# Performance work log

Measured on AMD Instinct MI355X. Metric: run time of the kernel, lower is better.

## Reference

```python
import math
import jax, jax.numpy as jnp
import numpy as np

B, L = 64, 25
FEAT, HEADS, LAYERS = 128, 8, 2
USER_N, POI_N, CAT_N = 5000, 10000, 400


def _autocorr(q, k, v):
    # q,k,v: [B,L,H,E] ; training-mode AutoCorrelation (self.training=True)
    Lq = q.shape[1]
    qp = jnp.transpose(q, (0, 2, 3, 1))  # [B,H,E,L]
    kp = jnp.transpose(k, (0, 2, 3, 1))
    vp = jnp.transpose(v, (0, 2, 3, 1))
    qf = jnp.fft.rfft(qp, axis=-1)
    kf = jnp.fft.rfft(kp, axis=-1)
    corr = jnp.fft.irfft(qf * jnp.conj(kf), n=Lq, axis=-1)  # [B,H,E,L]
    top_k = int(1 * math.log(Lq))  # factor=1 -> 3 for L=25
    mean_value = corr.mean(axis=(1, 2))  # [B,L]
    _, index = jax.lax.top_k(mean_value.mean(axis=0), top_k)  # [K], shared across batch
    weights = mean_value[:, index]  # [B,K]
    tmp_corr = jax.nn.softmax(weights, axis=-1)
    # roll(values, -delay) == gather at (t + delay) mod L
    gidx = (jnp.arange(Lq)[None, :] + index[:, None]) % Lq  # [K,L]
    patterns = vp[..., gidx]  # [B,H,E,K,L]
    agg = jnp.einsum('bhekl,bk->bhel', patterns, tmp_corr)  # weighted delay aggregation
    return jnp.transpose(agg, (0, 3, 1, 2))  # [B,L,H,E]


def _ac_layer(qx, kx, vx, w, b):
    # w: [4, d, d] torch-layout [out,in] for (q,k,v,out) projections; b: [4, d]
    Bq, Lq, d = qx.shape
    q = (qx @ w[0].T + b[0]).reshape(Bq, Lq, HEADS, -1)
    k = (kx @ w[1].T + b[1]).reshape(Bq, kx.shape[1], HEADS, -1)
    v = (vx @ w[2].T + b[2]).reshape(Bq, vx.shape[1], HEADS, -1)
    out = _autocorr(q, k, v).reshape(Bq, Lq, -1)
    return out @ w[3].T + b[3]


def setup_inputs() -> dict:
    key = jax.random.key(0)
    ks = jax.random.split(key, 16)
    d = FEAT
    inp = {
        'user': jax.random.randint(ks[0], (B, L), 0, USER_N),
        'poi': jax.random.randint(ks[1], (B, L), 0, POI_N),
        'cat': jax.random.randint(ks[2], (B, L), 0, CAT_N),
        'lat': jax.random.normal(ks[3], (B, L), jnp.float32),
        'lon': jax.random.normal(ks[4], (B, L), jnp.float32),
        'tod': jax.random.randint(ks[5], (B, L), 0, 24),
        'dow': jax.random.randint(ks[6], (B, L), 0, 7),
        'unixtime': jax.random.normal(ks[7], (B, L), jnp.float32),
        'user_emb': jax.random.normal(ks[8], (USER_N, d), jnp.float32) * 0.02,
        'poi_emb': jax.random.normal(ks[9], (POI_N, d), jnp.float32) * 0.02,
        'cat_emb': jax.random.normal(ks[10], (CAT_N, d), jnp.float32) * 0.02,
        'tod_emb': jax.random.normal(ks[11], (24, d), jnp.float32) * 0.02,
        'dow_emb': jax.random.normal(ks[12], (7, d), jnp.float32) * 0.02,
        'user_embc': jax.random.normal(jax.random.fold_in(ks[8], 1), (USER_N, d), jnp.float32) * 0.02,
        'tod_embc': jax.random.normal(jax.random.fold_in(ks[11], 1), (24, d), jnp.float32) * 0.02,
        'dow_embc': jax.random.normal(jax.random.fold_in(ks[12], 1), (7, d), jnp.float32) * 0.02,
        # W[layer, module(poi,cat,xpoi,xcat), proj(q,k,v,o), out, in]
        'W': jax.random.normal(ks[13], (LAYERS, 4, 4, d, d), jnp.float32) * (1.0 / math.sqrt(d)),
        'Bv': jnp.zeros((LAYERS, 4, 4, d), jnp.float32),
        'value_w': jax.random.normal(ks[14], (1, L), jnp.float32) * 0.1,
        'value_b': jnp.zeros((1,), jnp.float32),
        'distance_matrix': jax.random.uniform(ks[15], (POI_N, POI_N), jnp.float32) * 10.0,
    }
    return inp


def reference(user, poi, cat, lat, lon, tod, dow, unixtime,
              user_emb, poi_emb, cat_emb, tod_emb, dow_emb,
              user_embc, tod_embc, dow_embc,
              W, Bv, value_w, value_b, distance_matrix):
    x = user_emb[user] + poi_emb[poi] + tod_emb[tod] + dow_emb[dow]        # [B,L,d]
    xc = user_embc[user] + cat_emb[cat] + tod_embc[tod] + dow_embc[dow]   # [B,L,d]

    interval_dis = distance_matrix[poi]  # [B,L,P] row gather == index_select loop
    interval = jnp.exp(-interval_dis / (interval_dis.max() - interval_dis.min()))

    out, outc = x, xc
    for i in range(LAYERS):
        out = _ac_layer(out, out, out, W[i, 0], Bv[i, 0])
        outc = _ac_layer(outc, outc, outc, W[i, 1], Bv[i, 1])
        out = _ac_layer(out, outc, outc, W[i, 2], Bv[i, 2])
        outc = _ac_layer(outc, out, out, W[i, 3], Bv[i, 3])

    attn = jnp.einsum('pd,bld->bpl', poi_emb, out) * jnp.transpose(interval, (0, 2, 1))
    attn_cat = jnp.einsum('cd,bld->bcl', cat_emb, outc)
    pre_poi = (attn @ value_w.T + value_b)[..., 0]      # [B,P]
    pre_cat = (attn_cat @ value_w.T + value_b)[..., 0]  # [B,C]
    return pre_poi, pre_cat
```

## Files before the change

kernel.cpp:

```cpp
#include <hip/hip_runtime.h>
#include <hip/hip_bf16.h>

#define BB 64
#define LL 25
#define DD 128
#define BL 1600
#define POI_N 10000
#define CAT_N 400

__global__ __launch_bounds__(256) void embed_kernel(
    const int* __restrict__ user, const int* __restrict__ poi, const int* __restrict__ cat,
    const int* __restrict__ tod, const int* __restrict__ dow,
    const float* __restrict__ ue, const float* __restrict__ pe, const float* __restrict__ ce,
    const float* __restrict__ te, const float* __restrict__ de,
    const float* __restrict__ uec, const float* __restrict__ tec, const float* __restrict__ dec,
    float* __restrict__ x, float* __restrict__ xc, unsigned* __restrict__ mm)
{
    int idx = blockIdx.x * 256 + threadIdx.x;
    if (idx == 0) { mm[0] = 0u; mm[1] = 0x7f7fffffu; }
    int bl = idx >> 7, d = idx & 127;
    int u = user[bl], p = poi[bl], c = cat[bl], td = tod[bl], dw = dow[bl];
    x[idx]  = ue[u * DD + d] + pe[p * DD + d] + te[td * DD + d] + de[dw * DD + d];
    xc[idx] = uec[u * DD + d] + ce[c * DD + d] + tec[td * DD + d] + dec[dw * DD + d];
}

__global__ __launch_bounds__(256) void minmax_kernel(
    const int* __restrict__ poi, const float* __restrict__ Dm, unsigned* __restrict__ mm)
{
    int bl = blockIdx.x;
    const float4* r = (const float4*)(Dm + (size_t)poi[bl] * POI_N);
    float mx = -1e30f, mn = 1e30f;
    for (int i = threadIdx.x; i < POI_N / 4; i += 256) {
        float4 v4 = r[i];
        mx = fmaxf(mx, fmaxf(fmaxf(v4.x, v4.y), fmaxf(v4.z, v4.w)));
        mn = fminf(mn, fminf(fminf(v4.x, v4.y), fminf(v4.z, v4.w)));
    }
    for (int off = 32; off > 0; off >>= 1) {
        mx = fmaxf(mx, __shfl_down(mx, off));
        mn = fminf(mn, __shfl_down(mn, off));
    }
    __shared__ float smx[4], smn[4];
    int lid = threadIdx.x & 63, wid = threadIdx.x >> 6;
    if (lid == 0) { smx[wid] = mx; smn[wid] = mn; }
    __syncthreads();
    if (threadIdx.x == 0) {
        mx = fmaxf(fmaxf(smx[0], smx[1]), fmaxf(smx[2], smx[3]));
        mn = fminf(fminf(smn[0], smn[1]), fminf(smn[2], smn[3]));
        atomicMax(&mm[0], __float_as_uint(mx));
        atomicMin(&mm[1], __float_as_uint(mn));
    }
}

__global__ __launch_bounds__(256) void proj_kernel(
    const float* __restrict__ sq, const float* __restrict__ sk, const float* __restrict__ sv,
    const float* __restrict__ Wbase, const float* __restrict__ Bbase,
    float* __restrict__ q, float* __restrict__ k, float* __restrict__ v)
{
    int r = blockIdx.y;
    const float* src = (r == 0) ? sq : (r == 1 ? sk : sv);
    float* dst       = (r == 0) ? q  : (r == 1 ? k  : v);
    const float* Wm   = Wbase + r * DD * DD;
    const float* bias = Bbase + r * DD;
    int mbase = blockIdx.x * 32;
    __shared__ float sS[32][132];
    __shared__ float sWc[128][68];
    int t = threadIdx.x;

    for (int i = t; i < 32 * 32; i += 256) {
        int m = i >> 5, c = (i & 31) << 2;
        *(float4*)&sS[m][c] = *(const float4*)(src + (mbase + m) * DD + c);
    }
    __syncthreads();

    int nh = t & 31, mg = t >> 5;
    float acc[4][4] = {};
    for (int kb = 0; kb < 128; kb += 64) {
        for (int i = t; i < 128 * 16; i += 256) {
            int n = i >> 4, c = (i & 15) << 2;
            *(float4*)&sWc[n][c] = *(const float4*)(Wm + n * DD + kb + c);
        }
        __syncthreads();
#pragma unroll 4
        for (int kk = 0; kk < 64; kk += 4) {
            float4 a[4], w[4];
#pragma unroll
            for (int i2 = 0; i2 < 4; i2++) a[i2] = *(const float4*)&sS[mg * 4 + i2][kb + kk];
#pragma unroll
            for (int j = 0; j < 4; j++) w[j] = *(const float4*)&sWc[nh + 32 * j][kk];
#pragma unroll
            for (int i2 = 0; i2 < 4; i2++)
#pragma unroll
                for (int j = 0; j < 4; j++)
                    acc[i2][j] += a[i2].x * w[j].x + a[i2].y * w[j].y +
                                  a[i2].z * w[j].z + a[i2].w * w[j].w;
        }
        __syncthreads();
    }
#pragma unroll
    for (int i2 = 0; i2 < 4; i2++) {
        int m = mbase + mg * 4 + i2;
#pragma unroll
        for (int j = 0; j < 4; j++) {
            int n = nh + 32 * j;
            dst[m * DD + n] = acc[i2][j] + bias[n];
        }
    }
}

__global__ __launch_bounds__(256) void corr_kernel(
    const float* __restrict__ q, const float* __restrict__ k, float* __restrict__ mv)
{
    int b = blockIdx.x;
    __shared__ float sq[LL * DD], sk[LL * DD];
    __shared__ float rbuf[LL][4];
    int t = threadIdx.x;
    for (int i = t; i < 800; i += 256) {
        int c = i << 2;
        *(float4*)&sq[c] = *(const float4*)(q + b * LL * DD + c);
        *(float4*)&sk[c] = *(const float4*)(k + b * LL * DD + c);
    }
    __syncthreads();
    int lid = t & 63, wid = t >> 6;
    for (int tau = 0; tau < LL; tau++) {
        float s = 0.f;
        for (int e = t; e < LL * DD; e += 256) {
            int srow = e >> 7, d = e & 127;
            int qrow = srow + tau; if (qrow >= LL) qrow -= LL;
            s += sq[qrow * DD + d] * sk[e];
        }
        for (int off = 32; off > 0; off >>= 1) s += __shfl_down(s, off);
        if (lid == 0) rbuf[tau][wid] = s;
    }
    __syncthreads();
    if (t < LL)
        mv[b * LL + t] = (rbuf[t][0] + rbuf[t][1] + rbuf[t][2] + rbuf[t][3]) * (1.0f / 128.0f);
}

__global__ void topsm_kernel(const float* __restrict__ mv, float* __restrict__ tc,
                             int* __restrict__ idxout)
{
    __shared__ float sbm[LL];
    __shared__ int sidx[3];
    int t = threadIdx.x;
    if (t < LL) {
        float s = 0.f;
        for (int b = 0; b < BB; b++) s += mv[b * LL + t];
        sbm[t] = s;
    }
    __syncthreads();
    if (t == 0) {
        float loc[LL];
        for (int i = 0; i < LL; i++) loc[i] = sbm[i];
        for (int j = 0; j < 3; j++) {
            int bi = 0; float bvv = loc[0];
            for (int i = 1; i < LL; i++) if (loc[i] > bvv) { bvv = loc[i]; bi = i; }
            sidx[j] = bi; idxout[j] = bi; loc[bi] = -1e30f;
        }
    }
    __syncthreads();
    if (t < BB) {
        float w0 = mv[t * LL + sidx[0]];
        float w1 = mv[t * LL + sidx[1]];
        float w2 = mv[t * LL + sidx[2]];
        float m = fmaxf(w0, fmaxf(w1, w2));
        float e0 = expf(w0 - m), e1 = expf(w1 - m), e2 = expf(w2 - m);
        float inv = 1.0f / (e0 + e1 + e2);
        tc[t * 4 + 0] = e0 * inv; tc[t * 4 + 1] = e1 * inv; tc[t * 4 + 2] = e2 * inv;
    }
}

__global__ __launch_bounds__(256) void aggproj_kernel(
    const float* __restrict__ v, const float* __restrict__ tc, const int* __restrict__ idx3,
    const float* __restrict__ Wm, const float* __restrict__ bias, float* __restrict__ dst)
{
    int mbase = blockIdx.x * 32;
    __shared__ float sS[32][132];
    __shared__ float sWc[128][68];
    int t = threadIdx.x;
    int i0 = idx3[0], i1 = idx3[1], i2x = idx3[2];

    for (int i = t; i < 32 * 32; i += 256) {
        int m = i >> 5, c = (i & 31) << 2;
        int row = mbase + m;
        int b = row / LL, l = row - b * LL;
        int l0 = l + i0;  if (l0 >= LL) l0 -= LL;
        int l1 = l + i1;  if (l1 >= LL) l1 -= LL;
        int l2 = l + i2x; if (l2 >= LL) l2 -= LL;
        float w0 = tc[b * 4 + 0], w1 = tc[b * 4 + 1], w2 = tc[b * 4 + 2];
        float4 v0 = *(const float4*)(v + (b * LL + l0) * DD + c);
        float4 v1 = *(const float4*)(v + (b * LL + l1) * DD + c);
        float4 v2 = *(const float4*)(v + (b * LL + l2) * DD + c);
        float4 a;
        a.x = w0 * v0.x + w1 * v1.x + w2 * v2.x;
        a.y = w0 * v0.y + w1 * v1.y + w2 * v2.y;
        a.z = w0 * v0.z + w1 * v1.z + w2 * v2.z;
        a.w = w0 * v0.w + w1 * v1.w + w2 * v2.w;
        *(float4*)&sS[m][c] = a;
    }
    __syncthreads();

    int nh = t & 31, mg = t >> 5;
    float acc[4][4] = {};
    for (int kb = 0; kb < 128; kb += 64) {
        for (int i = t; i < 128 * 16; i += 256) {
            int n = i >> 4, c = (i & 15) << 2;
            *(float4*)&sWc[n][c] = *(const float4*)(Wm + n * DD + kb + c);
        }
        __syncthreads();
#pragma unroll 4
        for (int kk = 0; kk < 64; kk += 4) {
            float4 a[4], w[4];
#pragma unroll
            for (int ii = 0; ii < 4; ii++) a[ii] = *(const float4*)&sS[mg * 4 + ii][kb + kk];
#pragma unroll
            for (int j = 0; j < 4; j++) w[j] = *(const float4*)&sWc[nh + 32 * j][kk];
#pragma unroll
            for (int ii = 0; ii < 4; ii++)
#pragma unroll
                for (int j = 0; j < 4; j++)
                    acc[ii][j] += a[ii].x * w[j].x + a[ii].y * w[j].y +
                                  a[ii].z * w[j].z + a[ii].w * w[j].w;
        }
        __syncthreads();
    }
#pragma unroll
    for (int ii = 0; ii < 4; ii++) {
        int m = mbase + mg * 4 + ii;
#pragma unroll
        for (int j = 0; j < 4; j++) {
            int n = nh + 32 * j;
            dst[m * DD + n] = acc[ii][j] + bias[n];
        }
    }
}

__global__ __launch_bounds__(256) void precat_kernel(
    const float* __restrict__ outc, const float* __restrict__ cat_emb,
    const float* __restrict__ vw, const float* __restrict__ vbp, float* __restrict__ dstc)
{
    int b = blockIdx.x, t = threadIdx.x;
    __shared__ float y[DD];
    __shared__ float svw[LL];
    if (t < LL) svw[t] = vw[t];
    __syncthreads();
    if (t < DD) {
        float s = 0.f;
        for (int l = 0; l < LL; l++) s += svw[l] * outc[(b * LL + l) * DD + t];
        y[t] = s;
    }
    __syncthreads();
    float vb = vbp[0];
    for (int c = t; c < CAT_N; c += 256) {
        float s = 0.f;
        for (int d = 0; d < DD; d += 4) {
            float4 ce4 = *(const float4*)(cat_emb + c * DD + d);
            s += ce4.x * y[d] + ce4.y * y[d + 1] + ce4.z * y[d + 2] + ce4.w * y[d + 3];
        }
        dstc[b * CAT_N + c] = s + vb;
    }
}

__global__ __launch_bounds__(256) void prepoi_kernel(
    const float* __restrict__ outp, const float* __restrict__ poi_emb,
    const int* __restrict__ poi_idx, const float* __restrict__ Dm,
    const unsigned* __restrict__ mm, const float* __restrict__ vw,
    const float* __restrict__ vbp, float* __restrict__ dstp)
{
    int b = blockIdx.y;
    int pbase = blockIdx.x << 7;
    __shared__ float sO[LL][132];
    __shared__ float sPc[128][68];
    __shared__ float sS[LL][132];
    __shared__ float svw[LL];
    __shared__ int srow[LL];
    __shared__ float red[128];
    int t = threadIdx.x;

    for (int i = t; i < 800; i += 256) {
        int l = i >> 5, c = (i & 31) << 2;
        *(float4*)&sO[l][c] = *(const float4*)(outp + (b * LL + l) * DD + c);
    }
    if (t < LL) { svw[t] = vw[t]; srow[t] = poi_idx[b * LL + t]; }
    __syncthreads();

    int nh = t & 31, mg = t >> 5;
    float acc[4][4] = {};
    for (int kb = 0; kb < 128; kb += 64) {
        for (int i = t; i < 128 * 16; i += 256) {
            int p = i >> 4, c = (i & 15) << 2;
            float4 val = {0.f, 0.f, 0.f, 0.f};
            if (pbase + p < POI_N) val = *(const float4*)(poi_emb + (pbase + p) * DD + kb + c);
            *(float4*)&sPc[p][c] = val;
        }
        __syncthreads();
#pragma unroll 4
        for (int kk = 0; kk < 64; kk += 4) {
            float4 a0 = *(const float4*)&sO[mg][kb + kk];
            float4 a1 = *(const float4*)&sO[mg + 8][kb + kk];
            float4 a2 = *(const float4*)&sO[mg + 16][kb + kk];
            float4 a3 = {0.f, 0.f, 0.f, 0.f};
            if (mg == 0) a3 = *(const float4*)&sO[24][kb + kk];
#pragma unroll
            for (int j = 0; j < 4; j++) {
                float4 p4 = *(const float4*)&sPc[nh + 32 * j][kk];
                acc[j][0] += p4.x * a0.x + p4.y * a0.y + p4.z * a0.z + p4.w * a0.w;
                acc[j][1] += p4.x * a1.x + p4.y * a1.y + p4.z * a1.z + p4.w * a1.w;
                acc[j][2] += p4.x * a2.x + p4.y * a2.y + p4.z * a2.z + p4.w * a2.w;
                acc[j][3] += p4.x * a3.x + p4.y * a3.y + p4.z * a3.z + p4.w * a3.w;
            }
        }
        __syncthreads();
    }
#pragma unroll
    for (int j = 0; j < 4; j++) {
        int pl = nh + 32 * j;
        sS[mg][pl]      = acc[j][0];
        sS[mg + 8][pl]  = acc[j][1];
        sS[mg + 16][pl] = acc[j][2];
        if (mg == 0) sS[24][pl] = acc[j][3];
    }
    __syncthreads();

    float gmax = __uint_as_float(mm[0]);
    float gmin = __uint_as_float(mm[1]);
    float ninv = -1.0f / (gmax - gmin);
    int pp = t & 127, half = t >> 7;
    int p = pbase + pp;
    float s = 0.f;
    if (p < POI_N) {
        int l0 = half ? 13 : 0, l1 = half ? 25 : 13;
        for (int l = l0; l < l1; l++) {
            float dv = Dm[(size_t)srow[l] * POI_N + p];
            s += svw[l] * expf(dv * ninv) * sS[l][pp];
        }
    }
    if (half) red[pp] = s;
    __syncthreads();
    if (!half && p < POI_N)
        dstp[(size_t)b * POI_N + p] = s + red[pp] + vbp[0];
}

extern "C" void kernel_launch(void* const* d_in, const int* in_sizes, int n_in,
                              void* d_out, int out_size, void* d_ws, size_t ws_size,
                              hipStream_t stream)
{
    const int*   user = (const int*)d_in[0];
    const int*   poi  = (const int*)d_in[1];
    const int*   cat  = (const int*)d_in[2];
    const int*   tod  = (const int*)d_in[5];
    const int*   dow  = (const int*)d_in[6];
    const float* ue   = (const float*)d_in[8];
    const float* pe   = (const float*)d_in[9];
    const float* ce   = (const float*)d_in[10];
    const float* te   = (const float*)d_in[11];
    const float* de   = (const float*)d_in[12];
    const float* uec  = (const float*)d_in[13];
    const float* tec  = (const float*)d_in[14];
    const float* dec  = (const float*)d_in[15];
    const float* W    = (const float*)d_in[16];
    const float* Bv   = (const float*)d_in[17];
    const float* vw   = (const float*)d_in[18];
    const float* vb   = (const float*)d_in[19];
    const float* Dm   = (const float*)d_in[20];

    float* ws = (float*)d_ws;
    float* O0 = ws;
    float* C0 = ws + 204800;
    float* O1 = ws + 409600;
    float* C1 = ws + 614400;
    float* Q  = ws + 819200;
    float* Kb = ws + 1024000;
    float* V  = ws + 1228800;
    float* MV = ws + 1433600;
    float* TC = ws + 1435200;
    int*   IDX = (int*)(ws + 1435456);
    unsigned* MM = (unsigned*)(ws + 1435460);

    float* out_poi = (float*)d_out;
    float* out_cat = out_poi + BB * POI_N;

    embed_kernel<<<800, 256, 0, stream>>>(user, poi, cat, tod, dow,
                                          ue, pe, ce, te, de, uec, tec, dec, O0, C0, MM);
    minmax_kernel<<<BL, 256, 0, stream>>>(poi, Dm, MM);

    auto ac = [&](const float* qx, const float* kx, const float* vx, int i, int j, float* dstbuf) {
        const float* Wb = W + (size_t)((i * 4 + j) * 4) * DD * DD;
        const float* Bb = Bv + (size_t)((i * 4 + j) * 4) * DD;
        proj_kernel<<<dim3(50, 3), 256, 0, stream>>>(qx, kx, vx, Wb, Bb, Q, Kb, V);
        corr_kernel<<<BB, 256, 0, stream>>>(Q, Kb, MV);
        topsm_kernel<<<1, 256, 0, stream>>>(MV, TC, IDX);
        aggproj_kernel<<<50, 256, 0, stream>>>(V, TC, IDX, Wb + 3 * DD * DD, Bb + 3 * DD, dstbuf);
    };

    ac(O0, O0, O0, 0, 0, O1);
    ac(C0, C0, C0, 0, 1, C1);
    ac(O1, C1, C1, 0, 2, O0);
    ac(C1, O0, O0, 0, 3, C0);
    ac(O0, O0, O0, 1, 0, O1);
    ac(C0, C0, C0, 1, 1, C1);
    ac(O1, C1, C1, 1, 2, O0);
    ac(C1, O0, O0, 1, 3, C0);

    precat_kernel<<<BB, 256, 0, stream>>>(C0, ce, vw, vb, out_cat);
    prepoi_kernel<<<dim3(79, BB), 256, 0, stream>>>(O0, pe, poi, Dm, MM, vw, vb, out_poi);
}
```

Measured before the change: 1.201 ms.

## Fuse autocorrelation layer into two per-batch kernels and run independent layers concurrently

Replaces the four-kernel sequence per autocorrelation layer (projection, correlation, top-k/softmax, aggregation+output projection) with two per-batch kernels. The first computes Q and K in shared memory, does the circular correlation and accumulates the batch-mean via atomics. The second does top-k and softmax per block, projects V in shared memory, aggregates and applies the output projection. The two independent layers (out and outc paths) are launched together via a second grid dimension. This removes launches and global Q/K/V round-trips, but each block recomputes the top-k, and the atomic float sums make the ordering nondeterministic.

```diff
diff --git a/kernel.cpp b/kernel.cpp
--- a/kernel.cpp
+++ b/kernel.cpp
@@ -14,9 +14,11 @@
     const float* __restrict__ ue, const float* __restrict__ pe, const float* __restrict__ ce,
     const float* __restrict__ te, const float* __restrict__ de,
     const float* __restrict__ uec, const float* __restrict__ tec, const float* __restrict__ dec,
-    float* __restrict__ x, float* __restrict__ xc, unsigned* __restrict__ mm)
+    float* __restrict__ x, float* __restrict__ xc,
+    float* __restrict__ sbm_all, unsigned* __restrict__ mm)
 {
     int idx = blockIdx.x * 256 + threadIdx.x;
+    if (idx < 256) sbm_all[idx] = 0.0f;
     if (idx == 0) { mm[0] = 0u; mm[1] = 0x7f7fffffu; }
     int bl = idx >> 7, d = idx & 127;
     int u = user[bl], p = poi[bl], c = cat[bl], td = tod[bl], dw = dow[bl];
@@ -51,187 +53,170 @@
     }
 }
 
-__global__ __launch_bounds__(256) void proj_kernel(
-    const float* __restrict__ sq, const float* __restrict__ sk, const float* __restrict__ sv,
-    const float* __restrict__ Wbase, const float* __restrict__ Bbase,
-    float* __restrict__ q, float* __restrict__ k, float* __restrict__ v)
-{
-    int r = blockIdx.y;
-    const float* src = (r == 0) ? sq : (r == 1 ? sk : sv);
-    float* dst       = (r == 0) ? q  : (r == 1 ? k  : v);
-    const float* Wm   = Wbase + r * DD * DD;
-    const float* bias = Bbase + r * DD;
-    int mbase = blockIdx.x * 32;
-    __shared__ float sS[32][132];
-    __shared__ float sWc[128][68];
-    int t = threadIdx.x;
-
-    for (int i = t; i < 32 * 32; i += 256) {
-        int m = i >> 5, c = (i & 31) << 2;
-        *(float4*)&sS[m][c] = *(const float4*)(src + (mbase + m) * DD + c);
-    }
-    __syncthreads();
-
+template<bool TO_LDS>
+__device__ __forceinline__ void gemm25(const float (*sX)[132], float (*sW)[36],
+                                       const float* __restrict__ Wm,
+                                       const float* __restrict__ bias,
+                                       float (*sDst)[132], float* __restrict__ gRow, int t)
+{
     int nh = t & 31, mg = t >> 5;
     float acc[4][4] = {};
-    for (int kb = 0; kb < 128; kb += 64) {
-        for (int i = t; i < 128 * 16; i += 256) {
-            int n = i >> 4, c = (i & 15) << 2;
-            *(float4*)&sWc[n][c] = *(const float4*)(Wm + n * DD + kb + c);
+    for (int kb = 0; kb < DD; kb += 32) {
+        for (int i = t; i < 128 * 8; i += 256) {
+            int n = i >> 3, c = (i & 7) << 2;
+            *(float4*)&sW[n][c] = *(const float4*)(Wm + n * DD + kb + c);
         }
         __syncthreads();
-#pragma unroll 4
-        for (int kk = 0; kk < 64; kk += 4) {
-            float4 a[4], w[4];
-#pragma unroll
-            for (int i2 = 0; i2 < 4; i2++) a[i2] = *(const float4*)&sS[mg * 4 + i2][kb + kk];
-#pragma unroll
-            for (int j = 0; j < 4; j++) w[j] = *(const float4*)&sWc[nh + 32 * j][kk];
-#pragma unroll
-            for (int i2 = 0; i2 < 4; i2++)
-#pragma unroll
-                for (int j = 0; j < 4; j++)
-                    acc[i2][j] += a[i2].x * w[j].x + a[i2].y * w[j].y +
-                                  a[i2].z * w[j].z + a[i2].w * w[j].w;
+#pragma unroll
+        for (int kk = 0; kk < 32; kk += 4) {
+            float4 a0 = *(const float4*)&sX[mg][kb + kk];
+            float4 a1 = *(const float4*)&sX[mg + 8][kb + kk];
+            float4 a2 = *(const float4*)&sX[mg + 16][kb + kk];
+            float4 a3 = {0.f, 0.f, 0.f, 0.f};
+            if (mg == 0) a3 = *(const float4*)&sX[24][kb + kk];
+#pragma unroll
+            for (int j = 0; j < 4; j++) {
+                float4 w4 = *(const float4*)&sW[nh + 32 * j][kk];
+                acc[j][0] += w4.x * a0.x + w4.y * a0.y + w4.z * a0.z + w4.w * a0.w;
+                acc[j][1] += w4.x * a1.x + w4.y * a1.y + w4.z * a1.z + w4.w * a1.w;
+                acc[j][2] += w4.x * a2.x + w4.y * a2.y + w4.z * a2.z + w4.w * a2.w;
+                acc[j][3] += w4.x * a3.x + w4.y * a3.y + w4.z * a3.z + w4.w * a3.w;
+            }
         }
         __syncthreads();
     }
 #pragma unroll
-    for (int i2 = 0; i2 < 4; i2++) {
-        int m = mbase + mg * 4 + i2;
-#pragma unroll
-        for (int j = 0; j < 4; j++) {
-            int n = nh + 32 * j;
-            dst[m * DD + n] = acc[i2][j] + bias[n];
-        }
-    }
-}
-
-__global__ __launch_bounds__(256) void corr_kernel(
-    const float* __restrict__ q, const float* __restrict__ k, float* __restrict__ mv)
-{
-    int b = blockIdx.x;
-    __shared__ float sq[LL * DD], sk[LL * DD];
+    for (int j = 0; j < 4; j++) {
+        int n = nh + 32 * j;
+        float bj = bias[n];
+        if (TO_LDS) {
+            sDst[mg][n]      = acc[j][0] + bj;
+            sDst[mg + 8][n]  = acc[j][1] + bj;
+            sDst[mg + 16][n] = acc[j][2] + bj;
+            if (mg == 0) sDst[24][n] = acc[j][3] + bj;
+        } else {
+            gRow[mg * DD + n]        = acc[j][0] + bj;
+            gRow[(mg + 8) * DD + n]  = acc[j][1] + bj;
+            gRow[(mg + 16) * DD + n] = acc[j][2] + bj;
+            if (mg == 0) gRow[24 * DD + n] = acc[j][3] + bj;
+        }
+    }
+}
+
+struct AcArgs {
+    const float* qx; const float* kx; const float* vx;
+    const float* Wb;
+    const float* Bb;
+    float* dst;
+    float* mv;
+    float* sbm;
+};
+
+__global__ __launch_bounds__(256) void ac1_kernel(AcArgs a0, AcArgs a1)
+{
+    const AcArgs a = blockIdx.y ? a1 : a0;
+    int b = blockIdx.x, t = threadIdx.x;
+    __shared__ float sX[LL][132];
+    __shared__ float sW[128][36];
+    __shared__ float sQ[LL][132];
+    __shared__ float sK[LL][132];
     __shared__ float rbuf[LL][4];
-    int t = threadIdx.x;
-    for (int i = t; i < 800; i += 256) {
-        int c = i << 2;
-        *(float4*)&sq[c] = *(const float4*)(q + b * LL * DD + c);
-        *(float4*)&sk[c] = *(const float4*)(k + b * LL * DD + c);
-    }
-    __syncthreads();
+
+    for (int f = t; f < 800; f += 256) {
+        int l = f >> 5, c = (f & 31) << 2;
+        *(float4*)&sX[l][c] = *(const float4*)(a.qx + (b * LL + l) * DD + c);
+    }
+    __syncthreads();
+    gemm25<true>(sX, sW, a.Wb, a.Bb, sQ, nullptr, t);
+    for (int f = t; f < 800; f += 256) {
+        int l = f >> 5, c = (f & 31) << 2;
+        *(float4*)&sX[l][c] = *(const float4*)(a.kx + (b * LL + l) * DD + c);
+    }
+    __syncthreads();
+    gemm25<true>(sX, sW, a.Wb + DD * DD, a.Bb + DD, sK, nullptr, t);
+    __syncthreads();
+
     int lid = t & 63, wid = t >> 6;
     for (int tau = 0; tau < LL; tau++) {
         float s = 0.f;
         for (int e = t; e < LL * DD; e += 256) {
-            int srow = e >> 7, d = e & 127;
-            int qrow = srow + tau; if (qrow >= LL) qrow -= LL;
-            s += sq[qrow * DD + d] * sk[e];
+            int sr = e >> 7, d = e & 127;
+            int qr = sr + tau; if (qr >= LL) qr -= LL;
+            s += sQ[qr][d] * sK[sr][d];
         }
         for (int off = 32; off > 0; off >>= 1) s += __shfl_down(s, off);
         if (lid == 0) rbuf[tau][wid] = s;
     }
     __syncthreads();
-    if (t < LL)
-        mv[b * LL + t] = (rbuf[t][0] + rbuf[t][1] + rbuf[t][2] + rbuf[t][3]) * (1.0f / 128.0f);
-}
-
-__global__ void topsm_kernel(const float* __restrict__ mv, float* __restrict__ tc,
-                             int* __restrict__ idxout)
-{
-    __shared__ float sbm[LL];
+    if (t < LL) {
+        float v = (rbuf[t][0] + rbuf[t][1] + rbuf[t][2] + rbuf[t][3]) * (1.0f / 128.0f);
+        a.mv[b * LL + t] = v;
+        atomicAdd(&a.sbm[t], v);
+    }
+}
+
+__global__ __launch_bounds__(256) void ac2_kernel(AcArgs a0, AcArgs a1)
+{
+    const AcArgs a = blockIdx.y ? a1 : a0;
+    int b = blockIdx.x, t = threadIdx.x;
+    __shared__ float sX[LL][132];
+    __shared__ float sW[128][36];
+    __shared__ float sV[LL][132];
+    __shared__ float sA[LL][132];
     __shared__ int sidx[3];
-    int t = threadIdx.x;
-    if (t < LL) {
-        float s = 0.f;
-        for (int b = 0; b < BB; b++) s += mv[b * LL + t];
-        sbm[t] = s;
-    }
-    __syncthreads();
-    if (t == 0) {
-        float loc[LL];
-        for (int i = 0; i < LL; i++) loc[i] = sbm[i];
-        for (int j = 0; j < 3; j++) {
-            int bi = 0; float bvv = loc[0];
-            for (int i = 1; i < LL; i++) if (loc[i] > bvv) { bvv = loc[i]; bi = i; }
-            sidx[j] = bi; idxout[j] = bi; loc[bi] = -1e30f;
-        }
-    }
-    __syncthreads();
-    if (t < BB) {
-        float w0 = mv[t * LL + sidx[0]];
-        float w1 = mv[t * LL + sidx[1]];
-        float w2 = mv[t * LL + sidx[2]];
-        float m = fmaxf(w0, fmaxf(w1, w2));
-        float e0 = expf(w0 - m), e1 = expf(w1 - m), e2 = expf(w2 - m);
-        float inv = 1.0f / (e0 + e1 + e2);
-        tc[t * 4 + 0] = e0 * inv; tc[t * 4 + 1] = e1 * inv; tc[t * 4 + 2] = e2 * inv;
-    }
-}
-
-__global__ __launch_bounds__(256) void aggproj_kernel(
-    const float* __restrict__ v, const float* __restrict__ tc, const int* __restrict__ idx3,
-    const float* __restrict__ Wm, const float* __restrict__ bias, float* __restrict__ dst)
-{
-    int mbase = blockIdx.x * 32;
-    __shared__ float sS[32][132];
-    __shared__ float sWc[128][68];
-    int t = threadIdx.x;
-    int i0 = idx3[0], i1 = idx3[1], i2x = idx3[2];
-
-    for (int i = t; i < 32 * 32; i += 256) {
-        int m = i >> 5, c = (i & 31) << 2;
-        int row = mbase + m;
-        int b = row / LL, l = row - b * LL;
-        int l0 = l + i0;  if (l0 >= LL) l0 -= LL;
-        int l1 = l + i1;  if (l1 >= LL) l1 -= LL;
-        int l2 = l + i2x; if (l2 >= LL) l2 -= LL;
-        float w0 = tc[b * 4 + 0], w1 = tc[b * 4 + 1], w2 = tc[b * 4 + 2];
-        float4 v0 = *(const float4*)(v + (b * LL + l0) * DD + c);
-        float4 v1 = *(const float4*)(v + (b * LL + l1) * DD + c);
-        float4 v2 = *(const float4*)(v + (b * LL + l2) * DD + c);
-        float4 a;
-        a.x = w0 * v0.x + w1 * v1.x + w2 * v2.x;
-        a.y = w0 * v0.y + w1 * v1.y + w2 * v2.y;
-        a.z = w0 * v0.z + w1 * v1.z + w2 * v2.z;
-        a.w = w0 * v0.w + w1 * v1.w + w2 * v2.w;
-        *(float4*)&sS[m][c] = a;
-    }
-    __syncthreads();
-
-    int nh = t & 31, mg = t >> 5;
-    float acc[4][4] = {};
-    for (int kb = 0; kb < 128; kb += 64) {
-        for (int i = t; i < 128 * 16; i += 256) {
-            int n = i >> 4, c = (i & 15) << 2;
-            *(float4*)&sWc[n][c] = *(const float4*)(Wm + n * DD + kb + c);
-        }
-        __syncthreads();
-#pragma unroll 4
-        for (int kk = 0; kk < 64; kk += 4) {
-            float4 a[4], w[4];
-#pragma unroll
-            for (int ii = 0; ii < 4; ii++) a[ii] = *(const float4*)&sS[mg * 4 + ii][kb + kk];
-#pragma unroll
-            for (int j = 0; j < 4; j++) w[j] = *(const float4*)&sWc[nh + 32 * j][kk];
-#pragma unroll
-            for (int ii = 0; ii < 4; ii++)
-#pragma unroll
-                for (int j = 0; j < 4; j++)
-                    acc[ii][j] += a[ii].x * w[j].x + a[ii].y * w[j].y +
-                                  a[ii].z * w[j].z + a[ii].w * w[j].w;
-        }
-        __syncthreads();
-    }
-#pragma unroll
-    for (int ii = 0; ii < 4; ii++) {
-        int m = mbase + mg * 4 + ii;
-#pragma unroll
-        for (int j = 0; j < 4; j++) {
-            int n = nh + 32 * j;
-            dst[m * DD + n] = acc[ii][j] + bias[n];
-        }
-    }
+    __shared__ float sTc[3];
+
+    if (t < 64) {
+        float v = (t < LL) ? a.sbm[t] : -3e38f;
+        for (int r = 0; r < 3; r++) {
+            float bv = v; int bix = t;
+            for (int off = 32; off > 0; off >>= 1) {
+                float ov = __shfl_down(bv, off);
+                int   oi = __shfl_down(bix, off);
+                if (ov > bv) { bv = ov; bix = oi; }
+            }
+            bix = __shfl(bix, 0);
+            if (t == 0) sidx[r] = bix;
+            if (t == bix) v = -3e38f;
+        }
+        if (t == 0) {
+            float w0 = a.mv[b * LL + sidx[0]];
+            float w1 = a.mv[b * LL + sidx[1]];
+            float w2 = a.mv[b * LL + sidx[2]];
+            float m = fmaxf(w0, fmaxf(w1, w2));
+            float e0 = expf(w0 - m), e1 = expf(w1 - m), e2 = expf(w2 - m);
+            float inv = 1.0f / (e0 + e1 + e2);
+            sTc[0] = e0 * inv; sTc[1] = e1 * inv; sTc[2] = e2 * inv;
+        }
+    }
+    for (int f = t; f < 800; f += 256) {
+        int l = f >> 5, c = (f & 31) << 2;
+        *(float4*)&sX[l][c] = *(const float4*)(a.vx + (b * LL + l) * DD + c);
+    }
+    __syncthreads();
+    gemm25<true>(sX, sW, a.Wb + 2 * DD * DD, a.Bb + 2 * DD, sV, nullptr, t);
+    __syncthreads();
+
+    int i0 = sidx[0], i1 = sidx[1], i2 = sidx[2];
+    float w0 = sTc[0], w1 = sTc[1], w2 = sTc[2];
+    for (int f = t; f < 800; f += 256) {
+        int l = f >> 5, c = (f & 31) << 2;
+        int l0 = l + i0; if (l0 >= LL) l0 -= LL;
+        int l1 = l + i1; if (l1 >= LL) l1 -= LL;
+        int l2 = l + i2; if (l2 >= LL) l2 -= LL;
+        float4 v0 = *(const float4*)&sV[l0][c];
+        float4 v1 = *(const float4*)&sV[l1][c];
+        float4 v2 = *(const float4*)&sV[l2][c];
+        float4 r;
+        r.x = w0 * v0.x + w1 * v1.x + w2 * v2.x;
+        r.y = w0 * v0.y + w1 * v1.y + w2 * v2.y;
+        r.z = w0 * v0.z + w1 * v1.z + w2 * v2.z;
+        r.w = w0 * v0.w + w1 * v1.w + w2 * v2.w;
+        *(float4*)&sA[l][c] = r;
+    }
+    __syncthreads();
+    gemm25<false>(sA, sW, a.Wb + 3 * DD * DD, a.Bb + 3 * DD, nullptr,
+                  a.dst + b * LL * DD, t);
 }
 
 __global__ __launch_bounds__(256) void precat_kernel(
@@ -368,38 +353,42 @@
     float* C0 = ws + 204800;
     float* O1 = ws + 409600;
     float* C1 = ws + 614400;
-    float* Q  = ws + 819200;
-    float* Kb = ws + 1024000;
-    float* V  = ws + 1228800;
-    float* MV = ws + 1433600;
-    float* TC = ws + 1435200;
-    int*   IDX = (int*)(ws + 1435456);
-    unsigned* MM = (unsigned*)(ws + 1435460);
+    float* MV  = ws + 819200;
+    float* SBM = ws + 832000;
+    unsigned* MM = (unsigned*)(ws + 832256);
 
     float* out_poi = (float*)d_out;
     float* out_cat = out_poi + BB * POI_N;
 
     embed_kernel<<<800, 256, 0, stream>>>(user, poi, cat, tod, dow,
-                                          ue, pe, ce, te, de, uec, tec, dec, O0, C0, MM);
+                                          ue, pe, ce, te, de, uec, tec, dec,
+                                          O0, C0, SBM, MM);
     minmax_kernel<<<BL, 256, 0, stream>>>(poi, Dm, MM);
 
-    auto ac = [&](const float* qx, const float* kx, const float* vx, int i, int j, float* dstbuf) {
-        const float* Wb = W + (size_t)((i * 4 + j) * 4) * DD * DD;
-        const float* Bb = Bv + (size_t)((i * 4 + j) * 4) * DD;
-        proj_kernel<<<dim3(50, 3), 256, 0, stream>>>(qx, kx, vx, Wb, Bb, Q, Kb, V);
-        corr_kernel<<<BB, 256, 0, stream>>>(Q, Kb, MV);
-        topsm_kernel<<<1, 256, 0, stream>>>(MV, TC, IDX);
-        aggproj_kernel<<<50, 256, 0, stream>>>(V, TC, IDX, Wb + 3 * DD * DD, Bb + 3 * DD, dstbuf);
+    auto mk = [&](int inst, const float* qx, const float* kx, const float* vx,
+                  int i, int j, float* dstbuf) -> AcArgs {
+        AcArgs a;
+        a.qx = qx; a.kx = kx; a.vx = vx;
+        a.Wb = W + (size_t)((i * 4 + j) * 4) * DD * DD;
+        a.Bb = Bv + (size_t)((i * 4 + j) * 4) * DD;
+        a.dst = dstbuf;
+        a.mv  = MV + inst * BB * LL;
+        a.sbm = SBM + inst * 32;
+        return a;
     };
 
-    ac(O0, O0, O0, 0, 0, O1);
-    ac(C0, C0, C0, 0, 1, C1);
-    ac(O1, C1, C1, 0, 2, O0);
-    ac(C1, O0, O0, 0, 3, C0);
-    ac(O0, O0, O0, 1, 0, O1);
-    ac(C0, C0, C0, 1, 1, C1);
-    ac(O1, C1, C1, 1, 2, O0);
-    ac(C1, O0, O0, 1, 3, C0);
+    for (int i = 0; i < 2; i++) {
+        AcArgs A0 = mk(4 * i + 0, O0, O0, O0, i, 0, O1);
+        AcArgs A1 = mk(4 * i + 1, C0, C0, C0, i, 1, C1);
+        ac1_kernel<<<dim3(BB, 2), 256, 0, stream>>>(A0, A1);
+        ac2_kernel<<<dim3(BB, 2), 256, 0, stream>>>(A0, A1);
+        AcArgs A2 = mk(4 * i + 2, O1, C1, C1, i, 2, O0);
+        ac1_kernel<<<dim3(BB, 1), 256, 0, stream>>>(A2, A2);
+        ac2_kernel<<<dim3(BB, 1), 256, 0, stream>>>(A2, A2);
+        AcArgs A3 = mk(4 * i + 3, C1, O0, O0, i, 3, C0);
+        ac1_kernel<<<dim3(BB, 1), 256, 0, stream>>>(A3, A3);
+        ac2_kernel<<<dim3(BB, 1), 256, 0, stream>>>(A3, A3);
+    }
 
     precat_kernel<<<BB, 256, 0, stream>>>(C0, ce, vw, vb, out_cat);
     prepoi_kernel<<<dim3(79, BB), 256, 0, stream>>>(O0, pe, poi, Dm, MM, vw, vb, out_poi);
```

After: 1.267 ms. +5.4%, slower.
